# Optimization experiments

Hardware: AMD Instinct MI355X
Metric: run time of the kernel (lower is better)

## Reference

```python
import jax, jax.numpy as jnp
import numpy as np
import math

L, B, E, H = 1024, 4, 1024, 16
HD = E // H

def setup_inputs() -> dict:
    key = jax.random.key(0)
    ks = jax.random.split(key, 8)
    bound_in = math.sqrt(6.0 / (3 * E + E))  # xavier_uniform for [3E, E]
    bound_out = math.sqrt(1.0 / E)           # default Linear init
    return {
        "query": jax.random.normal(ks[0], (L, B, E), jnp.float32),
        "key": jax.random.normal(ks[1], (L, B, E), jnp.float32),
        "value": jax.random.normal(ks[2], (L, B, E), jnp.float32),
        "attn_mask": jnp.zeros((B, L, L), jnp.float32),
        "in_proj_weight": jax.random.uniform(ks[3], (3 * E, E), jnp.float32, -bound_in, bound_in),
        "in_proj_bias": jnp.zeros((3 * E,), jnp.float32),
        "out_proj_weight": jax.random.uniform(ks[4], (E, E), jnp.float32, -bound_out, bound_out),
        "out_proj_bias": jnp.zeros((E,), jnp.float32),
    }

def reference(query, key, value, attn_mask, in_proj_weight, in_proj_bias,
              out_proj_weight, out_proj_bias):
    # packed in-projection: q/k/v [L, B, E]
    q = query @ in_proj_weight[:E].T + in_proj_bias[:E]
    k = key @ in_proj_weight[E:2 * E].T + in_proj_bias[E:2 * E]
    v = value @ in_proj_weight[2 * E:].T + in_proj_bias[2 * E:]
    # [L, B, E] -> [B*H, L, HD]
    def to_heads(x):
        return x.reshape(L, B * H, HD).transpose(1, 0, 2)
    qh, kh, vh = to_heads(q), to_heads(k), to_heads(v)
    qh = qh / math.sqrt(HD)
    scores = jnp.einsum('bqd,bkd->bqk', qh, kh)  # [B*H, L, L]
    # per-batch mask repeated across heads: [B,L,L] -> [B*H,L,L]
    mask = jnp.repeat(attn_mask, H, axis=0)
    weights = jax.nn.softmax(scores + mask, axis=-1)
    out = jnp.einsum('bqk,bkd->bqd', weights, vh)  # [B*H, L, HD]
    out = out.transpose(1, 0, 2).reshape(L, B, E)
    attn_output = out @ out_proj_weight.T + out_proj_bias
    avg_weights = weights.reshape(B, H, L, L).mean(axis=1)
    return attn_output, avg_weights
```

## Files before the change

kernel.cpp:

```cpp
#include <hip/hip_runtime.h>
#include <hip/hip_bf16.h>
#include <cstdint>
#include <cstddef>

#define LL 1024
#define BB 4
#define EE 1024
#define HH 16
#define HD 64
#define NHEADS 64

typedef __bf16 bf16x8 __attribute__((ext_vector_type(8)));
typedef float f32x4 __attribute__((ext_vector_type(4)));
typedef unsigned short u16;
typedef unsigned char u8;

__device__ __forceinline__ u16 f2b(float f) {
  union { float f; unsigned int i; } v; v.f = f;
  unsigned int r = v.i + 0x7FFFu + ((v.i >> 16) & 1u);
  return (u16)(r >> 16);
}
__device__ __forceinline__ float fp8d(u8 b) {
  return __builtin_amdgcn_cvt_f32_fp8((int)b, 0);
}

__device__ __forceinline__ void gload16(const u16* g, u16* l) {
  __builtin_amdgcn_global_load_lds(
      (const __attribute__((address_space(1))) unsigned int*)(const void*)g,
      (__attribute__((address_space(3))) unsigned int*)(void*)l, 16, 0, 0);
}

#define CVT_TOTAL 5242880
__global__ __launch_bounds__(256)
void cvt_all(const float* __restrict__ q, const float* __restrict__ k,
             const float* __restrict__ v, const float* __restrict__ wi,
             const float* __restrict__ wo, const float* __restrict__ mask,
             u16* __restrict__ qb, u16* __restrict__ kb, u16* __restrict__ vb,
             u16* __restrict__ wib, u16* __restrict__ wob,
             unsigned int* __restrict__ emask) {
  int i = blockIdx.x * 256 + threadIdx.x;
  if (i >= CVT_TOTAL) return;
  if (i >= 4194304) {
    int off = i - 4194304;
    const float4 t = ((const float4*)mask)[off];
    int lo = __builtin_amdgcn_cvt_pk_fp8_f32(__expf(t.x), __expf(t.y), 0, false);
    int vv = __builtin_amdgcn_cvt_pk_fp8_f32(__expf(t.z), __expf(t.w), lo, true);
    emask[off] = (unsigned int)vv;
    return;
  }
  const float* s; u16* d; int off;
  if (i < 1048576)      { s = q;  d = qb;  off = i; }
  else if (i < 2097152) { s = k;  d = kb;  off = i - 1048576; }
  else if (i < 3145728) { s = v;  d = vb;  off = i - 2097152; }
  else if (i < 3932160) { s = wi; d = wib; off = i - 3145728; }
  else                  { s = wo; d = wob; off = i - 3932160; }
  const float4 t = ((const float4*)s)[off];
  u16 o[4] = { f2b(t.x), f2b(t.y), f2b(t.z), f2b(t.w) };
  *(uint2*)&d[(size_t)off * 4] = *(const uint2*)o;
}

__global__ __launch_bounds__(256, 3)
void gemm_in(const u16* __restrict__ A0, const u16* __restrict__ A1,
             const u16* __restrict__ A2, const u16* __restrict__ Bw,
             const float* __restrict__ bias,
             u16* __restrict__ Oq, u16* __restrict__ Ok, u16* __restrict__ Ov) {
  const int tid  = threadIdx.x;
  const int lane = tid & 63;
  const int wave = tid >> 6;
  const int quad = lane >> 4;
  const int l15  = lane & 15;
  const int wm = wave >> 1, wn = wave & 1;
  const int row0 = blockIdx.x * 128;
  const int col0 = blockIdx.y * 128;

  const int sec = col0 >> 10;
  const u16* A = (sec == 0) ? A0 : ((sec == 1) ? A1 : A2);

  __shared__ __align__(16) u16 lA[3][128][4][8];
  __shared__ __align__(16) u16 lB[3][128][4][8];

  f32x4 acc[4][4];
#pragma unroll
  for (int i = 0; i < 4; ++i)
#pragma unroll
    for (int j = 0; j < 4; ++j) { acc[i][j][0]=0.f; acc[i][j][1]=0.f; acc[i][j][2]=0.f; acc[i][j][3]=0.f; }

  auto stage = [&](int k0, int sbuf) {
#pragma unroll
    for (int p = 0; p < 2; ++p) {
      int lc = p * 256 + tid;
      int r = lc >> 2, gs = lc & 3;
      int gg = gs ^ ((r >> 1) & 3);
      gload16(A  + (size_t)(row0 + r) * EE + (k0 + (gg << 3)), &lA[sbuf][0][0][0] + lc * 8);
      gload16(Bw + (size_t)(col0 + r) * EE + (k0 + (gg << 3)), &lB[sbuf][0][0][0] + lc * 8);
    }
  };

  auto compute = [&](int cbuf) {
    const int gslot = quad ^ ((l15 >> 1) & 3);
    bf16x8 af[4], bfr[4];
#pragma unroll
    for (int i = 0; i < 4; ++i) af[i]  = *(const bf16x8*)&lA[cbuf][wm * 64 + i * 16 + l15][gslot][0];
#pragma unroll
    for (int j = 0; j < 4; ++j) bfr[j] = *(const bf16x8*)&lB[cbuf][wn * 64 + j * 16 + l15][gslot][0];
#pragma unroll
    for (int i = 0; i < 4; ++i)
#pragma unroll
      for (int j = 0; j < 4; ++j)
        acc[i][j] = __builtin_amdgcn_mfma_f32_16x16x32_bf16(af[i], bfr[j], acc[i][j], 0, 0, 0);
  };

  stage(0, 0);
  stage(32, 1);

  for (int it = 0; it < 31; ++it) {
    asm volatile("s_waitcnt vmcnt(4)" ::: "memory");
    __builtin_amdgcn_s_barrier();
    __builtin_amdgcn_sched_barrier(0);
    if (it < 30) stage((it + 2) * 32, (it + 2) % 3);
    compute(it % 3);
  }
  asm volatile("s_waitcnt vmcnt(0)" ::: "memory");
  __builtin_amdgcn_s_barrier();
  __builtin_amdgcn_sched_barrier(0);
  compute(31 % 3);

#pragma unroll
  for (int i = 0; i < 4; ++i) {
    const int grb = row0 + wm * 64 + i * 16 + quad * 4;
#pragma unroll
    for (int j = 0; j < 4; ++j) {
      const int gc = col0 + wn * 64 + j * 16 + l15;
      const float bv = bias[gc];
#pragma unroll
      for (int r = 0; r < 4; ++r) {
        float val = acc[i][j][r] + bv;
        const int gr = grb + r;
        const int l = gr >> 2, b = gr & 3;
        const int e = gc & 1023;
        const int h = e >> 6, d = e & 63;
        const int n = b * 16 + h;
        if (sec == 0)      Oq[((size_t)n * LL + l) * HD + d] = f2b(val * 0.125f);
        else if (sec == 1) Ok[((size_t)n * LL + l) * HD + d] = f2b(val);
        else               Ov[((size_t)n * HD + d) * LL + l] = f2b(val);
      }
    }
  }
}

__global__ __launch_bounds__(256, 2)
void gemm_out(const u16* __restrict__ A, const u16* __restrict__ Bw,
              const float* __restrict__ bias, float* __restrict__ Of) {
  const int tid  = threadIdx.x;
  const int lane = tid & 63;
  const int wave = tid >> 6;
  const int quad = lane >> 4;
  const int l15  = lane & 15;
  const int wm = wave >> 1, wn = wave & 1;
  const int row0 = blockIdx.x * 64;
  const int col0 = blockIdx.y * 128;

  __shared__ __align__(16) u16 lA[3][64][4][8];
  __shared__ __align__(16) u16 lB[3][128][4][8];

  f32x4 acc[2][4];
#pragma unroll
  for (int i = 0; i < 2; ++i)
#pragma unroll
    for (int j = 0; j < 4; ++j) { acc[i][j][0]=0.f; acc[i][j][1]=0.f; acc[i][j][2]=0.f; acc[i][j][3]=0.f; }

  auto stage = [&](int k0, int sbuf) {
    {
      int r = tid >> 2, gs = tid & 3;
      int gg = gs ^ ((r >> 1) & 3);
      gload16(A + (size_t)(row0 + r) * EE + (k0 + (gg << 3)), &lA[sbuf][0][0][0] + tid * 8);
    }
#pragma unroll
    for (int p = 0; p < 2; ++p) {
      int lc = p * 256 + tid;
      int rb = lc >> 2, gsb = lc & 3;
      int ggb = gsb ^ ((rb >> 1) & 3);
      gload16(Bw + (size_t)(col0 + rb) * EE + (k0 + (ggb << 3)), &lB[sbuf][0][0][0] + lc * 8);
    }
  };

  auto compute = [&](int cbuf) {
    const int gslot = quad ^ ((l15 >> 1) & 3);
    bf16x8 af[2], bfr[4];
#pragma unroll
    for (int i = 0; i < 2; ++i) af[i]  = *(const bf16x8*)&lA[cbuf][wm * 32 + i * 16 + l15][gslot][0];
#pragma unroll
    for (int j = 0; j < 4; ++j) bfr[j] = *(const bf16x8*)&lB[cbuf][wn * 64 + j * 16 + l15][gslot][0];
#pragma unroll
    for (int i = 0; i < 2; ++i)
#pragma unroll
      for (int j = 0; j < 4; ++j)
        acc[i][j] = __builtin_amdgcn_mfma_f32_16x16x32_bf16(af[i], bfr[j], acc[i][j], 0, 0, 0);
  };

  stage(0, 0);
  stage(32, 1);

  for (int it = 0; it < 31; ++it) {
    asm volatile("s_waitcnt vmcnt(3)" ::: "memory");
    __builtin_amdgcn_s_barrier();
    __builtin_amdgcn_sched_barrier(0);
    if (it < 30) stage((it + 2) * 32, (it + 2) % 3);
    compute(it % 3);
  }
  asm volatile("s_waitcnt vmcnt(0)" ::: "memory");
  __builtin_amdgcn_s_barrier();
  __builtin_amdgcn_sched_barrier(0);
  compute(31 % 3);

#pragma unroll
  for (int i = 0; i < 2; ++i) {
    const int grb = row0 + wm * 32 + i * 16 + quad * 4;
#pragma unroll
    for (int j = 0; j < 4; ++j) {
      const int gc = col0 + wn * 64 + j * 16 + l15;
      const float bv = bias[gc];
#pragma unroll
      for (int r = 0; r < 4; ++r)
        Of[(size_t)(grb + r) * EE + gc] = acc[i][j][r] + bv;
    }
  }
}

__global__ __launch_bounds__(512, 4)
void attn_fused(const u16* __restrict__ Qh, const u16* __restrict__ Kh,
                const u16* __restrict__ Vt, const u8* __restrict__ emask,
                float* __restrict__ rsbuf, u16* __restrict__ O) {
  const int tid = threadIdx.x, lane = tid & 63, wave = tid >> 6;
  const int quad = lane >> 4, l15 = lane & 15;
  const int n = blockIdx.x;
  const int q0 = blockIdx.y * 128;
  const int b = n >> 4, h = n & 15;
  const int qw = wave * 16;

  __shared__ __align__(16) u16 lQ[8][128][8];
  __shared__ __align__(16) u16 lK[2][8][64][8];
  __shared__ __align__(16) u16 lV[2][8][64][8];
  __shared__ __align__(16) u16 lW[128][72];

  const u16* Qb = Qh + ((size_t)n * LL + q0) * HD;
  const u16* Kb = Kh + (size_t)n * LL * HD;
  const u16* Vb = Vt + (size_t)n * HD * LL;

#pragma unroll
  for (int p = 0; p < 2; ++p) {
    int lc = p * 512 + tid;
    gload16(Qb + (lc & 127) * HD + ((lc >> 7) << 3), &lQ[0][0][0] + lc * 8);
  }
  gload16(Kb + (size_t)(tid & 63) * HD + ((tid >> 6) << 3), &lK[0][0][0][0] + tid * 8);
  gload16(Vb + (size_t)(tid & 63) * LL + ((tid >> 6) << 3),  &lV[0][0][0][0] + tid * 8);
  __syncthreads();

  bf16x8 aq0 = *(const bf16x8*)&lQ[quad][qw + l15][0];
  bf16x8 aq1 = *(const bf16x8*)&lQ[4 + quad][qw + l15][0];

  float sr[4] = {0.f,0.f,0.f,0.f};
  f32x4 ctx[4];
#pragma unroll
  for (int j = 0; j < 4; ++j) { ctx[j][0]=0.f; ctx[j][1]=0.f; ctx[j][2]=0.f; ctx[j][3]=0.f; }

  int buf = 0;
  for (int kc = 0; kc < 16; ++kc) {
    if (kc < 15) {
      gload16(Kb + (size_t)((kc + 1) * 64 + (tid & 63)) * HD + ((tid >> 6) << 3),
              &lK[buf ^ 1][0][0][0] + tid * 8);
      gload16(Vb + (size_t)(tid & 63) * LL + (kc + 1) * 64 + ((tid >> 6) << 3),
              &lV[buf ^ 1][0][0][0] + tid * 8);
    }

    f32x4 sc[4];
#pragma unroll
    for (int jk = 0; jk < 4; ++jk) {
      bf16x8 bk0 = *(const bf16x8*)&lK[buf][quad][jk * 16 + l15][0];
      bf16x8 bk1 = *(const bf16x8*)&lK[buf][4 + quad][jk * 16 + l15][0];
      f32x4 a; a[0]=0.f; a[1]=0.f; a[2]=0.f; a[3]=0.f;
      a = __builtin_amdgcn_mfma_f32_16x16x32_bf16(aq0, bk0, a, 0, 0, 0);
      a = __builtin_amdgcn_mfma_f32_16x16x32_bf16(aq1, bk1, a, 0, 0, 0);
      sc[jk] = a;
    }
#pragma unroll
    for (int r = 0; r < 4; ++r) {
      const int q = q0 + qw + quad * 4 + r;
      const u8* mp = emask + ((size_t)b << 20) + (size_t)q * LL + kc * 64 + l15;
      float ss = 0.0f;
#pragma unroll
      for (int jk = 0; jk < 4; ++jk) {
        float w = fp8d(mp[jk * 16]) * __expf(sc[jk][r]);
        ss += w;
        lW[qw + quad * 4 + r][jk * 16 + l15] = f2b(w);
      }
      sr[r] += ss;
    }

#pragma unroll
    for (int ks = 0; ks < 2; ++ks) {
      bf16x8 aw = *(const bf16x8*)&lW[qw + l15][ks * 32 + quad * 8];
#pragma unroll
      for (int j = 0; j < 4; ++j) {
        bf16x8 bv = *(const bf16x8*)&lV[buf][ks * 4 + quad][j * 16 + l15][0];
        ctx[j] = __builtin_amdgcn_mfma_f32_16x16x32_bf16(aw, bv, ctx[j], 0, 0, 0);
      }
    }

    __syncthreads();
    buf ^= 1;
  }

  float rs[4];
#pragma unroll
  for (int i = 0; i < 4; ++i) {
#pragma unroll
    for (int d = 1; d < 16; d <<= 1) sr[i] += __shfl_xor(sr[i], d);
    rs[i] = 1.0f / sr[i];
  }
#pragma unroll
  for (int j = 0; j < 4; ++j) {
    const int d = j * 16 + l15;
#pragma unroll
    for (int r = 0; r < 4; ++r) {
      const int l = q0 + qw + quad * 4 + r;
      O[((size_t)l * BB + b) * EE + h * 64 + d] = f2b(ctx[j][r] * rs[r]);
    }
  }
  if (l15 == 0) {
#pragma unroll
    for (int r = 0; r < 4; ++r) {
      const int q = q0 + qw + quad * 4 + r;
      rsbuf[n * LL + q] = rs[r];
    }
  }
}

__global__ __launch_bounds__(256, 2)
void attn_avg(const u16* __restrict__ Qh, const u16* __restrict__ Kh,
              const u8* __restrict__ emask, const float* __restrict__ rsbuf,
              float* __restrict__ avgout) {
  const int tid = threadIdx.x, lane = tid & 63, wave = tid >> 6;
  const int quad = lane >> 4, l15 = lane & 15;
  const int kc = blockIdx.x;
  const int q0 = blockIdx.y * 64;
  const int b = blockIdx.z;

  __shared__ __align__(16) u16 lQ[2][8][64][8];
  __shared__ __align__(16) u16 lK[2][8][128][8];

  float acc[8][4];
#pragma unroll
  for (int j = 0; j < 8; ++j)
#pragma unroll
    for (int r = 0; r < 4; ++r) acc[j][r] = 0.0f;

  const int qrb = q0 + wave * 16;

  {
    const int n0 = b * 16;
    const u16* Qb = Qh + ((size_t)n0 * LL + q0) * HD;
    const u16* Kb = Kh + ((size_t)n0 * LL + kc * 128) * HD;
#pragma unroll
    for (int p = 0; p < 2; ++p) {
      int lc = p * 256 + tid;
      gload16(Qb + (lc & 63) * HD + ((lc >> 6) << 3), &lQ[0][0][0][0] + lc * 8);
    }
#pragma unroll
    for (int p = 0; p < 4; ++p) {
      int lc = p * 256 + tid;
      gload16(Kb + (size_t)(lc & 127) * HD + ((lc >> 7) << 3), &lK[0][0][0][0] + lc * 8);
    }
  }

  for (int h = 0; h < 16; ++h) {
    const int buf = h & 1;
    __syncthreads();
    if (h < 15) {
      const int n1 = b * 16 + h + 1;
      const u16* Qb = Qh + ((size_t)n1 * LL + q0) * HD;
      const u16* Kb = Kh + ((size_t)n1 * LL + kc * 128) * HD;
#pragma unroll
      for (int p = 0; p < 2; ++p) {
        int lc = p * 256 + tid;
        gload16(Qb + (lc & 63) * HD + ((lc >> 6) << 3), &lQ[buf ^ 1][0][0][0] + lc * 8);
      }
#pragma unroll
      for (int p = 0; p < 4; ++p) {
        int lc = p * 256 + tid;
        gload16(Kb + (size_t)(lc & 127) * HD + ((lc >> 7) << 3), &lK[buf ^ 1][0][0][0] + lc * 8);
      }
    }

    const int n = b * 16 + h;
    float rs[4];
#pragma unroll
    for (int r = 0; r < 4; ++r) {
      const int q = qrb + quad * 4 + r;
      rs[r] = rsbuf[n * LL + q];
    }
    bf16x8 aq0 = *(const bf16x8*)&lQ[buf][quad][wave * 16 + l15][0];
    bf16x8 aq1 = *(const bf16x8*)&lQ[buf][4 + quad][wave * 16 + l15][0];
#pragma unroll
    for (int j = 0; j < 8; ++j) {
      bf16x8 bk0 = *(const bf16x8*)&lK[buf][quad][j * 16 + l15][0];
      bf16x8 bk1 = *(const bf16x8*)&lK[buf][4 + quad][j * 16 + l15][0];
      f32x4 a; a[0]=0.f; a[1]=0.f; a[2]=0.f; a[3]=0.f;
      a = __builtin_amdgcn_mfma_f32_16x16x32_bf16(aq0, bk0, a, 0, 0, 0);
      a = __builtin_amdgcn_mfma_f32_16x16x32_bf16(aq1, bk1, a, 0, 0, 0);
#pragma unroll
      for (int r = 0; r < 4; ++r) acc[j][r] += __expf(a[r]) * rs[r];
    }
  }
#pragma unroll
  for (int j = 0; j < 8; ++j) {
#pragma unroll
    for (int r = 0; r < 4; ++r) {
      const int q = qrb + quad * 4 + r;
      const int k = kc * 128 + j * 16 + l15;
      const size_t idx = ((size_t)b << 20) + (size_t)q * LL + k;
      avgout[idx] = acc[j][r] * 0.0625f * fp8d(emask[idx]);
    }
  }
}

extern "C" void kernel_launch(void* const* d_in, const int* in_sizes, int n_in,
                              void* d_out, int out_size, void* d_ws, size_t ws_size,
                              hipStream_t stream) {
  const float* query = (const float*)d_in[0];
  const float* key   = (const float*)d_in[1];
  const float* value = (const float*)d_in[2];
  const float* mask  = (const float*)d_in[3];
  const float* win   = (const float*)d_in[4];
  const float* bin   = (const float*)d_in[5];
  const float* wout  = (const float*)d_in[6];
  const float* bout  = (const float*)d_in[7];
  float* out = (float*)d_out;

  u16* qb    = (u16*)d_ws;
  u16* kb    = qb + (size_t)LL * BB * EE;
  u16* vb    = kb + (size_t)LL * BB * EE;
  u16* winb  = vb + (size_t)LL * BB * EE;
  u16* woutb = winb + (size_t)3 * EE * EE;
  u16* Qh = woutb + (size_t)EE * EE;
  u16* Kh = Qh + (size_t)NHEADS * LL * HD;
  u16* Vt = Kh + (size_t)NHEADS * LL * HD;
  u16* O  = Vt + (size_t)NHEADS * LL * HD;
  float* rsbuf = (float*)(O + (size_t)LL * BB * EE);
  u8* emask = (u8*)(rsbuf + NHEADS * LL);

  dim3 blk(256);
  cvt_all<<<dim3((CVT_TOTAL + 255) / 256), blk, 0, stream>>>(
      query, key, value, win, wout, mask, qb, kb, vb, winb, woutb,
      (unsigned int*)emask);
  gemm_in<<<dim3(32, 24), blk, 0, stream>>>(qb, kb, vb, winb, bin, Qh, Kh, Vt);
  attn_fused<<<dim3(64, 8), dim3(512), 0, stream>>>(Qh, Kh, Vt, emask, rsbuf, O);
  attn_avg<<<dim3(8, 16, 4), blk, 0, stream>>>(Qh, Kh, emask, rsbuf, out + (size_t)LL * BB * EE);
  gemm_out<<<dim3(64, 8), blk, 0, stream>>>(O, woutb, bout, out);
}
```

Before: 262.1 us.

## Interleave fp8 mask layout for dword loads and swizzle GEMM block order

The exp-mask is repacked so the four fp8 values a lane needs across the jk sub-tiles sit in one 32-bit word. Attention and avg kernels can then do a single dword load and unpack bytes with cvt_f32_fp8 selectors, instead of four scattered byte loads. Both GEMMs also remap block IDs into grouped tile order, which should improve L2 reuse of operand tiles across concurrently running blocks. The mask conversion kernel now reads the mask with strided, non-vectorized loads.

```diff
diff --git a/kernel.cpp b/kernel.cpp
--- a/kernel.cpp
+++ b/kernel.cpp
@@ -20,8 +20,8 @@
   unsigned int r = v.i + 0x7FFFu + ((v.i >> 16) & 1u);
   return (u16)(r >> 16);
 }
-__device__ __forceinline__ float fp8d(u8 b) {
-  return __builtin_amdgcn_cvt_f32_fp8((int)b, 0);
+__device__ __forceinline__ float fp8sel(unsigned int m4, int sel) {
+  return __builtin_amdgcn_cvt_f32_fp8((int)(m4 >> (sel * 8)), 0);
 }
 
 __device__ __forceinline__ void gload16(const u16* g, u16* l) {
@@ -42,10 +42,15 @@
   if (i >= CVT_TOTAL) return;
   if (i >= 4194304) {
     int off = i - 4194304;
-    const float4 t = ((const float4*)mask)[off];
-    int lo = __builtin_amdgcn_cvt_pk_fp8_f32(__expf(t.x), __expf(t.y), 0, false);
-    int vv = __builtin_amdgcn_cvt_pk_fp8_f32(__expf(t.z), __expf(t.w), lo, true);
-    emask[off] = (unsigned int)vv;
+    int l15 = off & 15, chunk = (off >> 4) & 15, bq = off >> 8;
+    const float* mrow = mask + (size_t)bq * 1024 + chunk * 64 + l15;
+    float e0 = __expf(mrow[0]);
+    float e1 = __expf(mrow[16]);
+    float e2 = __expf(mrow[32]);
+    float e3 = __expf(mrow[48]);
+    int lo = __builtin_amdgcn_cvt_pk_fp8_f32(e0, e1, 0, false);
+    int vv = __builtin_amdgcn_cvt_pk_fp8_f32(e2, e3, lo, true);
+    emask[(size_t)(bq * 16 + chunk) * 16 + l15] = (unsigned int)vv;
     return;
   }
   const float* s; u16* d; int off;
@@ -70,8 +75,10 @@
   const int quad = lane >> 4;
   const int l15  = lane & 15;
   const int wm = wave >> 1, wn = wave & 1;
-  const int row0 = blockIdx.x * 128;
-  const int col0 = blockIdx.y * 128;
+  const int bid = blockIdx.y * 32 + blockIdx.x;
+  const int lg  = (bid & 7) * 96 + (bid >> 3);
+  const int row0 = (lg & 31) * 128;
+  const int col0 = (lg >> 5) * 128;
 
   const int sec = col0 >> 10;
   const u16* A = (sec == 0) ? A0 : ((sec == 1) ? A1 : A2);
@@ -157,8 +164,10 @@
   const int quad = lane >> 4;
   const int l15  = lane & 15;
   const int wm = wave >> 1, wn = wave & 1;
-  const int row0 = blockIdx.x * 64;
-  const int col0 = blockIdx.y * 128;
+  const int bid = blockIdx.y * 64 + blockIdx.x;
+  const int lg  = (bid & 7) * 64 + (bid >> 3);
+  const int row0 = (lg & 63) * 64;
+  const int col0 = (lg >> 6) * 128;
 
   __shared__ __align__(16) u16 lA[3][64][4][8];
   __shared__ __align__(16) u16 lB[3][128][4][8];
@@ -246,6 +255,7 @@
   const u16* Qb = Qh + ((size_t)n * LL + q0) * HD;
   const u16* Kb = Kh + (size_t)n * LL * HD;
   const u16* Vb = Vt + (size_t)n * HD * LL;
+  const unsigned int* em32 = (const unsigned int*)emask;
 
 #pragma unroll
   for (int p = 0; p < 2; ++p) {
@@ -286,11 +296,16 @@
 #pragma unroll
     for (int r = 0; r < 4; ++r) {
       const int q = q0 + qw + quad * 4 + r;
-      const u8* mp = emask + ((size_t)b << 20) + (size_t)q * LL + kc * 64 + l15;
+      const unsigned int m4 = em32[(((size_t)b * 1024 + q) * 16 + kc) * 16 + l15];
+      float md[4];
+      md[0] = __builtin_amdgcn_cvt_f32_fp8((int)m4, 0);
+      md[1] = __builtin_amdgcn_cvt_f32_fp8((int)m4, 1);
+      md[2] = __builtin_amdgcn_cvt_f32_fp8((int)m4, 2);
+      md[3] = __builtin_amdgcn_cvt_f32_fp8((int)m4, 3);
       float ss = 0.0f;
 #pragma unroll
       for (int jk = 0; jk < 4; ++jk) {
-        float w = fp8d(mp[jk * 16]) * __expf(sc[jk][r]);
+        float w = md[jk] * __expf(sc[jk][r]);
         ss += w;
         lW[qw + quad * 4 + r][jk * 16 + l15] = f2b(w);
       }
@@ -356,6 +371,7 @@
     for (int r = 0; r < 4; ++r) acc[j][r] = 0.0f;
 
   const int qrb = q0 + wave * 16;
+  const unsigned int* em32 = (const unsigned int*)emask;
 
   {
     const int n0 = b * 16;
@@ -414,12 +430,14 @@
   }
 #pragma unroll
   for (int j = 0; j < 8; ++j) {
+    const int chunk = (kc << 1) + (j >> 2);
 #pragma unroll
     for (int r = 0; r < 4; ++r) {
       const int q = qrb + quad * 4 + r;
       const int k = kc * 128 + j * 16 + l15;
+      const unsigned int m4 = em32[(((size_t)b * 1024 + q) * 16 + chunk) * 16 + l15];
       const size_t idx = ((size_t)b << 20) + (size_t)q * LL + k;
-      avgout[idx] = acc[j][r] * 0.0625f * fp8d(emask[idx]);
+      avgout[idx] = acc[j][r] * 0.0625f * fp8sel(m4, j & 3);
     }
   }
 }
```

After: 270.4 us. 1.03x slower.
